# Performance work log

Hardware: AMD Instinct MI355X
Metric: run time of the kernel (lower is better)

Reference implementation:

```python
import jax, jax.numpy as jnp
import numpy as np

B, S, S2, H, L = 16, 512, 64, 128, 3
N_STEPS = 3


def setup_inputs() -> dict:
    key = jax.random.key(0)
    ks = jax.random.split(key, 20)
    lin = lambda k, fo, fi: jax.random.normal(k, (fo, fi), jnp.float32) * 0.02
    bound = 1.0 / np.sqrt(H)
    return {
        "states": jax.random.normal(ks[0], (B, S, H), jnp.float32),
        "state_mask": jnp.ones((B, S), jnp.float32),
        "actions": jax.random.normal(ks[1], (B, S2, H), jnp.float32),
        "actions_mask": jnp.ones((B, S2), jnp.float32),
        "adj_matrix": (jax.random.uniform(ks[2], (B, S, S)) < 0.05).astype(jnp.float32),
        "Wn": lin(ks[3], H, H), "bn": jnp.zeros((H,), jnp.float32),
        "Wu": lin(ks[4], H, 2 * H), "bu": jnp.zeros((H,), jnp.float32),
        "Wr": lin(ks[5], H, 2 * H), "br": jnp.zeros((H,), jnp.float32),
        "Wt": lin(ks[6], H, 2 * H), "bt": jnp.zeros((H,), jnp.float32),
        "Wa1": lin(ks[7], H, 2 * H), "ba1": jnp.zeros((H,), jnp.float32),
        "Wa2": lin(ks[8], 1, H), "ba2": jnp.zeros((1,), jnp.float32),
        "Wv": lin(ks[9], 1, H), "bv": jnp.zeros((1,), jnp.float32),
        "weight": jax.random.uniform(ks[10], (L, H, H), jnp.float32, -bound, bound),
        "bias": jax.random.uniform(ks[11], (L,), jnp.float32, -bound, bound),
    }


def reference(states, state_mask, actions, actions_mask, adj_matrix,
              Wn, bn, Wu, bu, Wr, br, Wt, bt, Wa1, ba1, Wa2, ba2,
              Wv, bv, weight, bias):
    # ---- GGNN gated propagation (n_steps=3, dropout inactive / eval mode) ----
    h = states
    for _ in range(N_STEPS):
        p = h @ Wn.T + bn                                  # [B,S,H]
        a = jnp.einsum('bij,bjk->bik', adj_matrix,
                       jnp.concatenate([p, h], -1))        # [B,S,2H]
        z = jax.nn.sigmoid(a @ Wu.T + bu)
        r = jax.nn.sigmoid(a @ Wr.T + br)
        h_hat = jnp.tanh(jnp.concatenate([p, r * h], -1) @ Wt.T + bt)
        h = (1.0 - z) * h + z * h_hat
    out = h                                                # [B,S,H]

    # ---- MLP pairwise attention: concat(q,k)@Wa1.T split into two GEMMs ----
    qp = actions @ Wa1[:, :H].T                            # [B,S2,H]
    kp = out @ Wa1[:, H:].T                                # [B,S,H]
    hpair = jax.nn.relu(qp[:, :, None, :] + kp[:, None, :, :] + ba1)  # [B,S2,S,H]
    scores = jax.nn.relu(jnp.einsum('bqkh,h->bqk', hpair, Wa2[0]) + ba2[0])
    mask = actions_mask[:, :, None] * state_mask[:, None, :]
    A = jnp.where(mask > 0, jnp.exp(scores), 0.0)          # masked_fill(-inf).exp()
    attn = A / jnp.maximum(A.sum(-1, keepdims=True), 2e-15)
    states_feat = jnp.einsum('bqk,bkh->bqh', attn, out)    # [B,S2,H]

    # ---- mean state semantic over action slots ----
    num = actions_mask.sum(1)[:, None, None]
    sem = states_feat.sum(1, keepdims=True) / num          # [B,1,H]

    # ---- dueling bilinear head ----
    adv = jnp.einsum('bsh,lhk,bsk->bsl', actions, weight, states_feat) + bias
    val = sem @ Wv.T + bv                                  # [B,1,1]
    q = val + adv - adv.mean(axis=(1, 2), keepdims=True)   # [B,S2,L]
    # actions_mask is all ones -> no_pad keeps every row
    return (q.reshape(-1, L),)
```

## Files before the change

### kernel.cpp

```cpp
#include <hip/hip_runtime.h>
#include <math.h>

constexpr int Bn  = 16;
constexpr int Sn  = 512;
constexpr int S2n = 64;
constexpr int Hn  = 128;
constexpr int Ln  = 3;
constexpr int NNZ_CAP = 128;

#define TID ((int)threadIdx.x)

typedef __attribute__((ext_vector_type(8))) short bf16x8;
typedef __attribute__((ext_vector_type(4))) float f32x4;

__device__ inline float wave_reduce_sum(float v) {
#pragma unroll
  for (int off = 32; off > 0; off >>= 1) v += __shfl_xor(v, off, 64);
  return v;
}

__device__ inline float block_reduce_sum(float v, float* red) {
  v = wave_reduce_sum(v);
  int w  = TID >> 6;
  int nw = (int)blockDim.x >> 6;
  if ((TID & 63) == 0) red[w] = v;
  __syncthreads();
  float s = 0.f;
  for (int i = 0; i < nw; ++i) s += red[i];
  __syncthreads();
  return s;
}

__device__ inline float sigm(float x) { return 1.f / (1.f + expf(-x)); }

__device__ inline unsigned short f2bf(float f) {
  unsigned int u = __float_as_uint(f);
  u = (u + 0x7fffu + ((u >> 16) & 1u)) >> 16;
  return (unsigned short)u;
}

__global__ __launch_bounds__(256) void prep_all(
    const float* __restrict__ adj,
    unsigned short* __restrict__ idx, int* __restrict__ cnts,
    const float* __restrict__ Wt, const float* __restrict__ Wa1,
    float* __restrict__ WtRT, float* __restrict__ Wa1T,
    const float* __restrict__ Wn, const float* __restrict__ Wu,
    const float* __restrict__ Wr, const float* __restrict__ bn,
    short* __restrict__ Bp,
    float* __restrict__ cu, float* __restrict__ cr, float* __restrict__ ct)
{
  __shared__ float t[32][33];
  __shared__ float Ws[2][128];
  __shared__ float bns[128];
  __shared__ float red[4];
  int bid = blockIdx.x;
  int tt = TID;
  int lane = tt & 63, wv = tt >> 6;

  if (bid < 2048) {
    int row = bid * 4 + wv;
    const float* ar = adj + (size_t)row * Sn;
    unsigned short* out = idx + (size_t)row * NNZ_CAP;
    int base = 0;
    for (int j0 = 0; j0 < Sn; j0 += 64) {
      float av = ar[j0 + lane];
      unsigned long long mask = __ballot(av != 0.f);
      int pos = __popcll(mask & ((1ull << lane) - 1ull));
      if (av != 0.f) out[base + pos] = (unsigned short)(j0 + lane);
      base += __popcll(mask);
    }
    if (lane == 0) cnts[row] = base;
    return;
  }
  if (bid < 2096) {
    int flat = bid - 2048;
    const float* src; float* dst; int k0, n0, woff;
    if (flat < 16) { src = Wt;  dst = WtRT; k0 = (flat & 3) * 32; n0 = (flat >> 2) * 32; woff = 128; }
    else { int f2 = flat - 16; src = Wa1; dst = Wa1T; k0 = (f2 & 7) * 32; n0 = (f2 >> 3) * 32; woff = 0; }
    int tx = tt & 31, ty = tt >> 5;
#pragma unroll
    for (int i = 0; i < 32; i += 8)
      t[ty + i][tx] = src[(size_t)(n0 + ty + i) * 256 + woff + k0 + tx];
    __syncthreads();
#pragma unroll
    for (int i = 0; i < 32; i += 8)
      dst[(size_t)(k0 + ty + i) * 128 + n0 + tx] = t[tx][ty + i];
    return;
  }
  int half = tt >> 7, tloc = tt & 127;
  int u = (bid - 2096) * 2 + half;
  int mat = u >> 7, n = u & 127;
  const float* W = (mat == 0) ? Wu : (mat == 1) ? Wr : Wt;
  float* cv = (mat == 0) ? cu : (mat == 1) ? cr : ct;
  Ws[half][tloc] = W[(size_t)n * 256 + tloc];
  if (tt < 128) bns[tt] = bn[tt];
  __syncthreads();
  float acc = 0.f;
#pragma unroll 4
  for (int c = 0; c < 128; ++c)
    acc = fmaf(Wn[(size_t)c * 128 + tloc], Ws[half][c], acc);
  if (mat < 2) acc += W[(size_t)n * 256 + 128 + tloc];
  int k = tloc;
  int id2 = ((mat * 8 + (n >> 4)) * 4 + (k >> 5)) * 512 +
            (((k & 31) >> 3) * 16 + (n & 15)) * 8 + (k & 7);
  Bp[id2] = (short)f2bf(acc);
  float pv = bns[tloc] * Ws[half][tloc];
  pv = wave_reduce_sum(pv);
  if (lane == 0) red[wv] = pv;
  __syncthreads();
  if (tloc == 0) cv[n] = red[half * 2] + red[half * 2 + 1];
}

__global__ __launch_bounds__(256) void gemm_gf(
    const float* __restrict__ h, const short* __restrict__ Bp,
    const float* __restrict__ ctv, float* __restrict__ g)
{
  int w = TID >> 6, l = TID & 63;
  int x = blockIdx.x;
  int b = x & 15, tt = x >> 4;
  int r0 = b * 512 + tt * 64 + w * 16;
  int mat = blockIdx.y;
  const float* abase = h + (size_t)(r0 + (l & 15)) * 128 + (l >> 4) * 8;
  bf16x8 a[4];
#pragma unroll
  for (int kc = 0; kc < 4; ++kc) {
    float4 f0 = *(const float4*)(abase + kc * 32);
    float4 f1 = *(const float4*)(abase + kc * 32 + 4);
    bf16x8 v;
    v[0] = (short)f2bf(f0.x); v[1] = (short)f2bf(f0.y);
    v[2] = (short)f2bf(f0.z); v[3] = (short)f2bf(f0.w);
    v[4] = (short)f2bf(f1.x); v[5] = (short)f2bf(f1.y);
    v[6] = (short)f2bf(f1.z); v[7] = (short)f2bf(f1.w);
    a[kc] = v;
  }
  f32x4 acc[8];
#pragma unroll
  for (int nt = 0; nt < 8; ++nt) acc[nt] = (f32x4){0.f, 0.f, 0.f, 0.f};
  const short* bbase = Bp + (size_t)(mat * 8) * 4 * 512 + l * 8;
#pragma unroll
  for (int nt = 0; nt < 8; ++nt)
#pragma unroll
    for (int kc = 0; kc < 4; ++kc) {
      bf16x8 bb = *(const bf16x8*)(bbase + (nt * 4 + kc) * 512);
      acc[nt] = __builtin_amdgcn_mfma_f32_16x16x32_bf16(a[kc], bb, acc[nt], 0, 0, 0);
    }
  int col0 = l & 15, rb2 = (l >> 4) * 4;
  float* gout = g + (size_t)(r0 + rb2) * 384 + mat * 128 + col0;
#pragma unroll
  for (int nt = 0; nt < 8; ++nt) {
    float cadd = (mat == 2) ? ctv[nt * 16 + col0] : 0.f;
#pragma unroll
    for (int r = 0; r < 4; ++r)
      gout[(size_t)r * 384 + nt * 16] = acc[nt][r] + cadd;
  }
}

__global__ __launch_bounds__(256) void adj_gate(
    const unsigned short* __restrict__ idx, const int* __restrict__ cnts,
    const float* __restrict__ g, const float* __restrict__ h,
    const float* __restrict__ cu, const float* __restrict__ cr,
    const float* __restrict__ bu, const float* __restrict__ br,
    float* __restrict__ z, float* __restrict__ rh)
{
  int bid = blockIdx.x;
  int b = bid & 15, tl = bid >> 4;
  int wid = TID >> 6, lane = TID & 63;
  int i = tl * 4 + wid;
  size_t row = (size_t)b * Sn + i;
  int c = (lane < 32) ? 4 * lane : 128 + 4 * (lane - 32);
  const float* gb = g + (size_t)b * Sn * 384 + c;
  const unsigned short* ix = idx + row * NNZ_CAP;
  int cnt = cnts[row];
  float4 acc = {0.f, 0.f, 0.f, 0.f};
  int n = 0;
  for (; n + 8 <= cnt; n += 8) {
    ushort4 ja = *(const ushort4*)(ix + n);
    ushort4 jb = *(const ushort4*)(ix + n + 4);
    float4 x0 = *(const float4*)(gb + (size_t)ja.x * 384);
    float4 x1 = *(const float4*)(gb + (size_t)ja.y * 384);
    float4 x2 = *(const float4*)(gb + (size_t)ja.z * 384);
    float4 x3 = *(const float4*)(gb + (size_t)ja.w * 384);
    float4 x4 = *(const float4*)(gb + (size_t)jb.x * 384);
    float4 x5 = *(const float4*)(gb + (size_t)jb.y * 384);
    float4 x6 = *(const float4*)(gb + (size_t)jb.z * 384);
    float4 x7 = *(const float4*)(gb + (size_t)jb.w * 384);
    acc.x += ((x0.x + x1.x) + (x2.x + x3.x)) + ((x4.x + x5.x) + (x6.x + x7.x));
    acc.y += ((x0.y + x1.y) + (x2.y + x3.y)) + ((x4.y + x5.y) + (x6.y + x7.y));
    acc.z += ((x0.z + x1.z) + (x2.z + x3.z)) + ((x4.z + x5.z) + (x6.z + x7.z));
    acc.w += ((x0.w + x1.w) + (x2.w + x3.w)) + ((x4.w + x5.w) + (x6.w + x7.w));
  }
  for (; n + 4 <= cnt; n += 4) {
    ushort4 jj = *(const ushort4*)(ix + n);
    float4 x0 = *(const float4*)(gb + (size_t)jj.x * 384);
    float4 x1 = *(const float4*)(gb + (size_t)jj.y * 384);
    float4 x2 = *(const float4*)(gb + (size_t)jj.z * 384);
    float4 x3 = *(const float4*)(gb + (size_t)jj.w * 384);
    acc.x += (x0.x + x1.x) + (x2.x + x3.x);
    acc.y += (x0.y + x1.y) + (x2.y + x3.y);
    acc.z += (x0.z + x1.z) + (x2.z + x3.z);
    acc.w += (x0.w + x1.w) + (x2.w + x3.w);
  }
  for (; n < cnt; ++n) {
    int j = ix[n];
    float4 x = *(const float4*)(gb + (size_t)j * 384);
    acc.x += x.x; acc.y += x.y; acc.z += x.z; acc.w += x.w;
  }
  float d = (float)cnt;
  int cc = (lane < 32) ? 4 * lane : 4 * (lane - 32);
  const float* cvp = (lane < 32) ? cu : cr;
  const float* bvp = (lane < 32) ? bu : br;
  float4 cv = *(const float4*)(cvp + cc);
  float4 bv = *(const float4*)(bvp + cc);
  float4 sg;
  sg.x = sigm(acc.x + d * cv.x + bv.x);
  sg.y = sigm(acc.y + d * cv.y + bv.y);
  sg.z = sigm(acc.z + d * cv.z + bv.z);
  sg.w = sigm(acc.w + d * cv.w + bv.w);
  if (lane < 32) {
    *(float4*)(z + row * 128 + cc) = sg;
  } else {
    float4 hv = *(const float4*)(h + row * 128 + cc);
    sg.x *= hv.x; sg.y *= hv.y; sg.z *= hv.z; sg.w *= hv.w;
    *(float4*)(rh + row * 128 + cc) = sg;
  }
}

__global__ __launch_bounds__(256) void gemm_hh(
    const float* __restrict__ rh, const float* __restrict__ g,
    const float* __restrict__ WtRT, const float* __restrict__ bt,
    const float* __restrict__ z, const float* __restrict__ h_in,
    float* __restrict__ h_out,
    const float* __restrict__ WeT, float* __restrict__ e_out,
    const float* __restrict__ qX, const float* __restrict__ qWT,
    float* __restrict__ qY)
{
  __shared__ float Xs[16 * 128];
  int bid = blockIdx.x;
  int t = TID;
  int c4 = (t & 31) * 4;
  int rb = (t >> 5) * 2;

  if (bid >= 512) {
    int r0 = (bid - 512) * 16;
    const float* xsrc = qX + (size_t)r0 * 128;
    for (int i = t; i < 512; i += 256)
      ((float4*)Xs)[i] = ((const float4*)xsrc)[i];
    __syncthreads();
    float acc[2][4] = {};
#pragma unroll 4
    for (int k = 0; k < 128; k += 4) {
      const float* wk = qWT + (size_t)k * 128 + c4;
      float4 w0 = *(const float4*)(wk);
      float4 w1 = *(const float4*)(wk + 128);
      float4 w2 = *(const float4*)(wk + 256);
      float4 w3 = *(const float4*)(wk + 384);
#pragma unroll
      for (int r = 0; r < 2; ++r) {
        float4 x = *(const float4*)&Xs[(rb + r) * 128 + k];
        acc[r][0] = fmaf(x.x, w0.x, acc[r][0]); acc[r][0] = fmaf(x.y, w1.x, acc[r][0]);
        acc[r][0] = fmaf(x.z, w2.x, acc[r][0]); acc[r][0] = fmaf(x.w, w3.x, acc[r][0]);
        acc[r][1] = fmaf(x.x, w0.y, acc[r][1]); acc[r][1] = fmaf(x.y, w1.y, acc[r][1]);
        acc[r][1] = fmaf(x.z, w2.y, acc[r][1]); acc[r][1] = fmaf(x.w, w3.y, acc[r][1]);
        acc[r][2] = fmaf(x.x, w0.z, acc[r][2]); acc[r][2] = fmaf(x.y, w1.z, acc[r][2]);
        acc[r][2] = fmaf(x.z, w2.z, acc[r][2]); acc[r][2] = fmaf(x.w, w3.z, acc[r][2]);
        acc[r][3] = fmaf(x.x, w0.w, acc[r][3]); acc[r][3] = fmaf(x.y, w1.w, acc[r][3]);
        acc[r][3] = fmaf(x.z, w2.w, acc[r][3]); acc[r][3] = fmaf(x.w, w3.w, acc[r][3]);
      }
    }
#pragma unroll
    for (int r = 0; r < 2; ++r) {
      float4 v = {acc[r][0], acc[r][1], acc[r][2], acc[r][3]};
      *(float4*)(qY + (size_t)(r0 + rb + r) * 128 + c4) = v;
    }
    return;
  }

  int b = bid & 15, tile = bid >> 4;
  int r0 = b * 512 + tile * 16;
  const float* xsrc = rh + (size_t)r0 * 128;
  for (int i = t; i < 512; i += 256)
    ((float4*)Xs)[i] = ((const float4*)xsrc)[i];
  __syncthreads();
  float acc[2][4] = {};
#pragma unroll 4
  for (int k = 0; k < 128; k += 4) {
    const float* wk = WtRT + (size_t)k * 128 + c4;
    float4 w0 = *(const float4*)(wk);
    float4 w1 = *(const float4*)(wk + 128);
    float4 w2 = *(const float4*)(wk + 256);
    float4 w3 = *(const float4*)(wk + 384);
#pragma unroll
    for (int r = 0; r < 2; ++r) {
      float4 x = *(const float4*)&Xs[(rb + r) * 128 + k];
      acc[r][0] = fmaf(x.x, w0.x, acc[r][0]); acc[r][0] = fmaf(x.y, w1.x, acc[r][0]);
      acc[r][0] = fmaf(x.z, w2.x, acc[r][0]); acc[r][0] = fmaf(x.w, w3.x, acc[r][0]);
      acc[r][1] = fmaf(x.x, w0.y, acc[r][1]); acc[r][1] = fmaf(x.y, w1.y, acc[r][1]);
      acc[r][1] = fmaf(x.z, w2.y, acc[r][1]); acc[r][1] = fmaf(x.w, w3.y, acc[r][1]);
      acc[r][2] = fmaf(x.x, w0.z, acc[r][2]); acc[r][2] = fmaf(x.y, w1.z, acc[r][2]);
      acc[r][2] = fmaf(x.z, w2.z, acc[r][2]); acc[r][2] = fmaf(x.w, w3.z, acc[r][2]);
      acc[r][3] = fmaf(x.x, w0.w, acc[r][3]); acc[r][3] = fmaf(x.y, w1.w, acc[r][3]);
      acc[r][3] = fmaf(x.z, w2.w, acc[r][3]); acc[r][3] = fmaf(x.w, w3.w, acc[r][3]);
    }
  }
  float4 btv = *(const float4*)(bt + c4);
  float hn[2][4];
#pragma unroll
  for (int r = 0; r < 2; ++r) {
    size_t row = r0 + rb + r;
    float4 gt = *(const float4*)(g + row * 384 + 256 + c4);
    float4 hv = *(const float4*)(h_in + row * 128 + c4);
    float4 zv = *(const float4*)(z + row * 128 + c4);
    hn[r][0] = hv.x + zv.x * (tanhf(acc[r][0] + gt.x + btv.x) - hv.x);
    hn[r][1] = hv.y + zv.y * (tanhf(acc[r][1] + gt.y + btv.y) - hv.y);
    hn[r][2] = hv.z + zv.z * (tanhf(acc[r][2] + gt.z + btv.z) - hv.z);
    hn[r][3] = hv.w + zv.w * (tanhf(acc[r][3] + gt.w + btv.w) - hv.w);
    float4 o = {hn[r][0], hn[r][1], hn[r][2], hn[r][3]};
    *(float4*)(h_out + row * 128 + c4) = o;
  }
  if (WeT) {
    __syncthreads();
#pragma unroll
    for (int r = 0; r < 2; ++r) {
      float4 o = {hn[r][0], hn[r][1], hn[r][2], hn[r][3]};
      *(float4*)&Xs[(rb + r) * 128 + c4] = o;
    }
    __syncthreads();
    float acc2[2][4] = {};
#pragma unroll 4
    for (int k = 0; k < 128; k += 4) {
      const float* wk = WeT + (size_t)k * 128 + c4;
      float4 w0 = *(const float4*)(wk);
      float4 w1 = *(const float4*)(wk + 128);
      float4 w2 = *(const float4*)(wk + 256);
      float4 w3 = *(const float4*)(wk + 384);
#pragma unroll
      for (int r = 0; r < 2; ++r) {
        float4 x = *(const float4*)&Xs[(rb + r) * 128 + k];
        acc2[r][0] = fmaf(x.x, w0.x, acc2[r][0]); acc2[r][0] = fmaf(x.y, w1.x, acc2[r][0]);
        acc2[r][0] = fmaf(x.z, w2.x, acc2[r][0]); acc2[r][0] = fmaf(x.w, w3.x, acc2[r][0]);
        acc2[r][1] = fmaf(x.x, w0.y, acc2[r][1]); acc2[r][1] = fmaf(x.y, w1.y, acc2[r][1]);
        acc2[r][1] = fmaf(x.z, w2.y, acc2[r][1]); acc2[r][1] = fmaf(x.w, w3.y, acc2[r][1]);
        acc2[r][2] = fmaf(x.x, w0.z, acc2[r][2]); acc2[r][2] = fmaf(x.y, w1.z, acc2[r][2]);
        acc2[r][2] = fmaf(x.z, w2.z, acc2[r][2]); acc2[r][2] = fmaf(x.w, w3.z, acc2[r][2]);
        acc2[r][3] = fmaf(x.x, w0.w, acc2[r][3]); acc2[r][3] = fmaf(x.y, w1.w, acc2[r][3]);
        acc2[r][3] = fmaf(x.z, w2.w, acc2[r][3]); acc2[r][3] = fmaf(x.w, w3.w, acc2[r][3]);
      }
    }
#pragma unroll
    for (int r = 0; r < 2; ++r) {
      float4 v = {acc2[r][0], acc2[r][1], acc2[r][2], acc2[r][3]};
      *(float4*)(e_out + (size_t)(r0 + rb + r) * 128 + c4) = v;
    }
  }
}

__global__ __launch_bounds__(256) void scores_exp_v3(
    const float* __restrict__ qp, const float* __restrict__ kp,
    const float* __restrict__ ba1, const float* __restrict__ Wa2,
    const float* __restrict__ ba2, const float* __restrict__ am,
    const float* __restrict__ smk, float* __restrict__ E)
{
  constexpr int KT = 32, QT = 32;
  __shared__ float qs[QT][132];
  __shared__ float ks[KT][132];
  __shared__ float w2s[128];
  __shared__ float es[QT][33];
  int b = blockIdx.z, kt = blockIdx.x * KT, qt = blockIdx.y * QT;
  const float* qsrc = qp + ((size_t)b * S2n + qt) * Hn;
  for (int f = TID; f < QT * 32; f += 256) {
    int q = f >> 5, g = f & 31;
    float4 v  = ((const float4*)qsrc)[f];
    float4 bb = ((const float4*)ba1)[g];
    v.x += bb.x; v.y += bb.y; v.z += bb.z; v.w += bb.w;
    *(float4*)&qs[q][4 * g] = v;
  }
  const float* ksrc = kp + ((size_t)b * Sn + kt) * Hn;
  for (int f = TID; f < KT * 32; f += 256) {
    int k = f >> 5, g = f & 31;
    *(float4*)&ks[k][4 * g] = ((const float4*)ksrc)[f];
  }
  if (TID < 128) w2s[TID] = Wa2[TID];
  __syncthreads();
  const int q0 = (TID & 15) * 2;
  const int k0 = (TID >> 4) * 2;
  float acc[2][2] = {};
#pragma unroll 4
  for (int h = 0; h < 128; ++h) {
    float w  = w2s[h];
    float kv0 = ks[k0][h], kv1 = ks[k0 + 1][h];
    float qv0 = qs[q0][h], qv1 = qs[q0 + 1][h];
    acc[0][0] = fmaf(fmaxf(qv0 + kv0, 0.f), w, acc[0][0]);
    acc[0][1] = fmaf(fmaxf(qv0 + kv1, 0.f), w, acc[0][1]);
    acc[1][0] = fmaf(fmaxf(qv1 + kv0, 0.f), w, acc[1][0]);
    acc[1][1] = fmaf(fmaxf(qv1 + kv1, 0.f), w, acc[1][1]);
  }
  float b2 = ba2[0];
#pragma unroll
  for (int i = 0; i < 2; ++i) {
    float amq = am[b * S2n + qt + q0 + i];
#pragma unroll
    for (int j = 0; j < 2; ++j) {
      float m = amq * smk[b * Sn + kt + k0 + j];
      float s = fmaxf(acc[i][j] + b2, 0.f);
      es[q0 + i][k0 + j] = (m > 0.f) ? expf(s) : 0.f;
    }
  }
  __syncthreads();
  float* Eb = E + ((size_t)b * S2n + qt) * Sn + kt;
  for (int f = TID; f < QT * KT; f += 256) {
    int q = f >> 5, kin = f & 31;
    Eb[(size_t)q * Sn + kin] = es[q][kin];
  }
}

__global__ __launch_bounds__(256) void fused_fg2(
    const float* __restrict__ E, const float* __restrict__ h,
    const float* __restrict__ actions, const float* __restrict__ weight,
    const float* __restrict__ bias, float* __restrict__ sf,
    float* __restrict__ adv)
{
  __shared__ float Es[2][512];
  __shared__ float red[4];
  __shared__ float sfs[2][128];
  __shared__ float acts[2][128];
  __shared__ float redl[12];
  int bid = blockIdx.x;
  int b = bid & 15, qpair = bid >> 4;
  int t = TID, lane = t & 63, wv = t >> 6;
  int half = t >> 7, tloc = t & 127;
  int q = qpair * 2 + half;
  size_t rowq = (size_t)b * S2n + q;
  const float* Erow = E + rowq * Sn;
  for (int i = tloc; i < Sn; i += 128) Es[half][i] = Erow[i];
  __syncthreads();
  float part = Es[half][tloc] + Es[half][tloc + 128] +
               Es[half][tloc + 256] + Es[half][tloc + 384];
  part = wave_reduce_sum(part);
  if (lane == 0) red[wv] = part;
  __syncthreads();
  float scale = 1.f / fmaxf(red[half * 2] + red[half * 2 + 1], 2e-15f);

  const float* ob = h + (size_t)b * Sn * Hn + tloc;
  float a0 = 0.f, a1 = 0.f, a2 = 0.f, a3 = 0.f;
#pragma unroll 4
  for (int k = 0; k < Sn; k += 4) {
    float e0 = Es[half][k],     h0 = ob[(size_t)k * Hn];
    float e1 = Es[half][k + 1], h1 = ob[(size_t)(k + 1) * Hn];
    float e2 = Es[half][k + 2], h2 = ob[(size_t)(k + 2) * Hn];
    float e3 = Es[half][k + 3], h3 = ob[(size_t)(k + 3) * Hn];
    a0 = fmaf(e0, h0, a0);
    a1 = fmaf(e1, h1, a1);
    a2 = fmaf(e2, h2, a2);
    a3 = fmaf(e3, h3, a3);
  }
  float sfv = ((a0 + a1) + (a2 + a3)) * scale;
  sf[rowq * Hn + tloc] = sfv;
  sfs[half][tloc]  = sfv;
  acts[half][tloc] = actions[rowq * Hn + tloc];
  __syncthreads();

  float tmp[3] = {0.f, 0.f, 0.f};
#pragma unroll
  for (int l = 0; l < Ln; ++l) {
    const float* wr = weight + ((size_t)l * Hn + tloc) * Hn;
#pragma unroll 4
    for (int k = 0; k < Hn; k += 4) {
      float4 wv4 = *(const float4*)(wr + k);
      tmp[l] = fmaf(wv4.x, sfs[half][k],     tmp[l]);
      tmp[l] = fmaf(wv4.y, sfs[half][k + 1], tmp[l]);
      tmp[l] = fmaf(wv4.z, sfs[half][k + 2], tmp[l]);
      tmp[l] = fmaf(wv4.w, sfs[half][k + 3], tmp[l]);
    }
  }
  float av = acts[half][tloc];
  float p0 = wave_reduce_sum(av * tmp[0]);
  float p1 = wave_reduce_sum(av * tmp[1]);
  float p2 = wave_reduce_sum(av * tmp[2]);
  if (lane == 0) {
    redl[wv * 3 + 0] = p0;
    redl[wv * 3 + 1] = p1;
    redl[wv * 3 + 2] = p2;
  }
  __syncthreads();
  if (tloc < Ln) {
    float tot = redl[(half * 2) * 3 + tloc] + redl[(half * 2 + 1) * 3 + tloc];
    adv[rowq * Ln + tloc] = tot + bias[tloc];
  }
}

__global__ __launch_bounds__(256) void final2_kernel(
    const float* __restrict__ sf, const float* __restrict__ am,
    const float* __restrict__ Wv, const float* __restrict__ bv,
    const float* __restrict__ adv, float* __restrict__ outq)
{
  __shared__ float red[4];
  int b = blockIdx.x, t = TID;
  float num = 0.f;
  for (int i = 0; i < S2n; ++i) num += am[b * S2n + i];
  float pv = 0.f;
  if (t < Hn) {
    float s = 0.f;
    const float* sb = sf + (size_t)b * S2n * Hn + t;
    for (int q = 0; q < S2n; ++q) s += sb[(size_t)q * Hn];
    pv = Wv[t] * (s / num);
  }
  float val = block_reduce_sum(pv, red) + bv[0];
  const float* advb = adv + (size_t)b * S2n * Ln;
  float pa   = (t < S2n * Ln) ? advb[t] : 0.f;
  float mean = block_reduce_sum(pa, red) / (float)(S2n * Ln);
  for (int i = t; i < S2n * Ln; i += 256)
    outq[(size_t)b * S2n * Ln + i] = val + advb[i] - mean;
}

extern "C" void kernel_launch(void* const* d_in, const int* in_sizes, int n_in,
                              void* d_out, int out_size, void* d_ws, size_t ws_size,
                              hipStream_t stream)
{
  const float* states       = (const float*)d_in[0];
  const float* state_mask   = (const float*)d_in[1];
  const float* actions      = (const float*)d_in[2];
  const float* actions_mask = (const float*)d_in[3];
  const float* adj          = (const float*)d_in[4];
  const float* Wn  = (const float*)d_in[5];
  const float* bn  = (const float*)d_in[6];
  const float* Wu  = (const float*)d_in[7];
  const float* bu  = (const float*)d_in[8];
  const float* Wr  = (const float*)d_in[9];
  const float* br  = (const float*)d_in[10];
  const float* Wt  = (const float*)d_in[11];
  const float* bt  = (const float*)d_in[12];
  const float* Wa1 = (const float*)d_in[13];
  const float* ba1 = (const float*)d_in[14];
  const float* Wa2 = (const float*)d_in[15];
  const float* ba2 = (const float*)d_in[16];
  const float* Wv  = (const float*)d_in[17];
  const float* bvp = (const float*)d_in[18];
  const float* weight = (const float*)d_in[19];
  const float* bias   = (const float*)d_in[20];

  float* ws   = (float*)d_ws;
  float* h    = ws;
  float* g    = ws + (1 << 20);
  float* zp   = ws + 4 * (1 << 20);
  float* rh   = ws + 5 * (1 << 20);
  float* kp   = ws + 6 * (1 << 20);
  float* qp   = ws + 7 * (1 << 20);
  float* E    = ws + 8 * (1 << 20);
  float* sfb  = ws + 9 * (1 << 20);
  float* adv  = sfb + 262144;
  float* aux  = ws + 10 * (1 << 20);
  float* WtRT = aux;
  float* Wa1T = WtRT + 16384;
  float* cu   = Wa1T + 32768;
  float* cr   = cu + 128;
  float* ct   = cr + 128;
  short* Bp   = (short*)(ws + 12 * (1 << 20));
  unsigned short* idx = (unsigned short*)(ws + 13 * (1 << 20));
  int* cnts   = (int*)(ws + 14 * (1 << 20));

  prep_all<<<2048 + 48 + 192, 256, 0, stream>>>(
      adj, idx, cnts, Wt, Wa1, WtRT, Wa1T,
      Wn, Wu, Wr, bn, Bp, cu, cr, ct);

  for (int step = 0; step < 3; ++step) {
    const float* hin = (step == 0) ? states : h;
    gemm_gf<<<dim3(128, 3), 256, 0, stream>>>(hin, Bp, ct, g);
    adj_gate<<<2048, 256, 0, stream>>>(idx, cnts, g, hin,
                                       cu, cr, bu, br, zp, rh);
    int grid = (step == 0) ? 512 + 64 : 512;
    gemm_hh<<<grid, 256, 0, stream>>>(
        rh, g, WtRT, bt, zp, hin, h,
        step == 2 ? Wa1T + 16384 : nullptr, kp,
        actions, Wa1T, qp);
  }

  scores_exp_v3<<<dim3(Sn / 32, 2, Bn), 256, 0, stream>>>(
      qp, kp, ba1, Wa2, ba2, actions_mask, state_mask, E);
  fused_fg2<<<512, 256, 0, stream>>>(E, h, actions, weight,
                                     bias, sfb, adv);
  final2_kernel<<<Bn, 256, 0, stream>>>(sfb, actions_mask, Wv, bvp, adv,
                                        (float*)d_out);
}
```

Baseline: 173.3 us.

## Fuse pairwise score/exp computation into attention aggregation kernel

Merges the score+exp kernel into the attention aggregation kernel, so each block computes the exp-scores for its two query rows directly in shared memory instead of writing and re-reading the E matrix through global memory. This removes one launch and the E round trip. In exchange, each thread now reads kp rows straight from global memory with a strided per-thread access pattern instead of through a shared tile. Each kp row is also reloaded by all 32 query-pair blocks of a batch, which reduces data reuse.

```diff
diff --git a/kernel.cpp b/kernel.cpp
--- a/kernel.cpp
+++ b/kernel.cpp
@@ -354,71 +354,17 @@
   }
 }
 
-__global__ __launch_bounds__(256) void scores_exp_v3(
+__global__ __launch_bounds__(256) void fused_attn(
     const float* __restrict__ qp, const float* __restrict__ kp,
     const float* __restrict__ ba1, const float* __restrict__ Wa2,
     const float* __restrict__ ba2, const float* __restrict__ am,
-    const float* __restrict__ smk, float* __restrict__ E)
-{
-  constexpr int KT = 32, QT = 32;
-  __shared__ float qs[QT][132];
-  __shared__ float ks[KT][132];
-  __shared__ float w2s[128];
-  __shared__ float es[QT][33];
-  int b = blockIdx.z, kt = blockIdx.x * KT, qt = blockIdx.y * QT;
-  const float* qsrc = qp + ((size_t)b * S2n + qt) * Hn;
-  for (int f = TID; f < QT * 32; f += 256) {
-    int q = f >> 5, g = f & 31;
-    float4 v  = ((const float4*)qsrc)[f];
-    float4 bb = ((const float4*)ba1)[g];
-    v.x += bb.x; v.y += bb.y; v.z += bb.z; v.w += bb.w;
-    *(float4*)&qs[q][4 * g] = v;
-  }
-  const float* ksrc = kp + ((size_t)b * Sn + kt) * Hn;
-  for (int f = TID; f < KT * 32; f += 256) {
-    int k = f >> 5, g = f & 31;
-    *(float4*)&ks[k][4 * g] = ((const float4*)ksrc)[f];
-  }
-  if (TID < 128) w2s[TID] = Wa2[TID];
-  __syncthreads();
-  const int q0 = (TID & 15) * 2;
-  const int k0 = (TID >> 4) * 2;
-  float acc[2][2] = {};
-#pragma unroll 4
-  for (int h = 0; h < 128; ++h) {
-    float w  = w2s[h];
-    float kv0 = ks[k0][h], kv1 = ks[k0 + 1][h];
-    float qv0 = qs[q0][h], qv1 = qs[q0 + 1][h];
-    acc[0][0] = fmaf(fmaxf(qv0 + kv0, 0.f), w, acc[0][0]);
-    acc[0][1] = fmaf(fmaxf(qv0 + kv1, 0.f), w, acc[0][1]);
-    acc[1][0] = fmaf(fmaxf(qv1 + kv0, 0.f), w, acc[1][0]);
-    acc[1][1] = fmaf(fmaxf(qv1 + kv1, 0.f), w, acc[1][1]);
-  }
-  float b2 = ba2[0];
-#pragma unroll
-  for (int i = 0; i < 2; ++i) {
-    float amq = am[b * S2n + qt + q0 + i];
-#pragma unroll
-    for (int j = 0; j < 2; ++j) {
-      float m = amq * smk[b * Sn + kt + k0 + j];
-      float s = fmaxf(acc[i][j] + b2, 0.f);
-      es[q0 + i][k0 + j] = (m > 0.f) ? expf(s) : 0.f;
-    }
-  }
-  __syncthreads();
-  float* Eb = E + ((size_t)b * S2n + qt) * Sn + kt;
-  for (int f = TID; f < QT * KT; f += 256) {
-    int q = f >> 5, kin = f & 31;
-    Eb[(size_t)q * Sn + kin] = es[q][kin];
-  }
-}
-
-__global__ __launch_bounds__(256) void fused_fg2(
-    const float* __restrict__ E, const float* __restrict__ h,
+    const float* __restrict__ smk, const float* __restrict__ h,
     const float* __restrict__ actions, const float* __restrict__ weight,
     const float* __restrict__ bias, float* __restrict__ sf,
     float* __restrict__ adv)
 {
+  __shared__ float qs[2][128];
+  __shared__ float w2s[128];
   __shared__ float Es[2][512];
   __shared__ float red[4];
   __shared__ float sfs[2][128];
@@ -428,11 +374,39 @@
   int b = bid & 15, qpair = bid >> 4;
   int t = TID, lane = t & 63, wv = t >> 6;
   int half = t >> 7, tloc = t & 127;
-  int q = qpair * 2 + half;
-  size_t rowq = (size_t)b * S2n + q;
-  const float* Erow = E + rowq * Sn;
-  for (int i = tloc; i < Sn; i += 128) Es[half][i] = Erow[i];
-  __syncthreads();
+  int q0g = qpair * 2;
+
+  qs[half][tloc] = qp[((size_t)b * S2n + q0g + half) * Hn + tloc] + ba1[tloc];
+  if (t < 128) w2s[t] = Wa2[t];
+  __syncthreads();
+
+  {
+    float b2  = ba2[0];
+    float am0 = am[b * S2n + q0g];
+    float am1 = am[b * S2n + q0g + 1];
+    const float* kb0 = kp + ((size_t)b * Sn + t) * Hn;
+    const float* kb1 = kb0 + 256 * Hn;
+    float s00 = 0.f, s01 = 0.f, s10 = 0.f, s11 = 0.f;
+#pragma unroll 4
+    for (int hh = 0; hh < 128; ++hh) {
+      float w   = w2s[hh];
+      float kv0 = kb0[hh], kv1 = kb1[hh];
+      float q0v = qs[0][hh], q1v = qs[1][hh];
+      s00 = fmaf(fmaxf(q0v + kv0, 0.f), w, s00);
+      s10 = fmaf(fmaxf(q1v + kv0, 0.f), w, s10);
+      s01 = fmaf(fmaxf(q0v + kv1, 0.f), w, s01);
+      s11 = fmaf(fmaxf(q1v + kv1, 0.f), w, s11);
+    }
+    float m0 = smk[b * Sn + t];
+    float m1 = smk[b * Sn + t + 256];
+    Es[0][t]       = (am0 * m0 > 0.f) ? expf(fmaxf(s00 + b2, 0.f)) : 0.f;
+    Es[0][t + 256] = (am0 * m1 > 0.f) ? expf(fmaxf(s01 + b2, 0.f)) : 0.f;
+    Es[1][t]       = (am1 * m0 > 0.f) ? expf(fmaxf(s10 + b2, 0.f)) : 0.f;
+    Es[1][t + 256] = (am1 * m1 > 0.f) ? expf(fmaxf(s11 + b2, 0.f)) : 0.f;
+  }
+  __syncthreads();
+
+  size_t rowq = (size_t)b * S2n + q0g + half;
   float part = Es[half][tloc] + Es[half][tloc + 128] +
                Es[half][tloc + 256] + Es[half][tloc + 384];
   part = wave_reduce_sum(part);
@@ -545,7 +519,6 @@
   float* rh   = ws + 5 * (1 << 20);
   float* kp   = ws + 6 * (1 << 20);
   float* qp   = ws + 7 * (1 << 20);
-  float* E    = ws + 8 * (1 << 20);
   float* sfb  = ws + 9 * (1 << 20);
   float* adv  = sfb + 262144;
   float* aux  = ws + 10 * (1 << 20);
@@ -574,10 +547,9 @@
         actions, Wa1T, qp);
   }
 
-  scores_exp_v3<<<dim3(Sn / 32, 2, Bn), 256, 0, stream>>>(
-      qp, kp, ba1, Wa2, ba2, actions_mask, state_mask, E);
-  fused_fg2<<<512, 256, 0, stream>>>(E, h, actions, weight,
-                                     bias, sfb, adv);
+  fused_attn<<<512, 256, 0, stream>>>(qp, kp, ba1, Wa2, ba2,
+                                      actions_mask, state_mask, h,
+                                      actions, weight, bias, sfb, adv);
   final2_kernel<<<Bn, 256, 0, stream>>>(sfb, actions_mask, Wv, bvp, adv,
                                         (float*)d_out);
 }
```

Result: slower. 188.1 us (+8.5%).
